# Optimization experiments

Hardware: AMD Instinct MI355X
Metric: run time of the kernel (lower is better)

Reference implementation:

```python
import jax, jax.numpy as jnp
import numpy as np

DIM = 1024
NUM_HEADS = 16
HEAD_DIM = DIM // NUM_HEADS
B, L = 4, 2048


def setup_inputs() -> dict:
    key = jax.random.key(0)
    ks = jax.random.split(key, 7)
    x = jax.random.normal(ks[0], (B, L, DIM), dtype=jnp.float32)
    cos_emb = jax.random.uniform(ks[1], (L, HEAD_DIM), dtype=jnp.float32)
    sin_emb = jax.random.uniform(ks[2], (L, HEAD_DIM), dtype=jnp.float32)
    # nn.Linear params: weight [out, in], bias [out]
    qkv_w = jax.random.normal(ks[3], (3 * DIM, DIM), dtype=jnp.float32) * (DIM ** -0.5)
    qkv_b = jnp.zeros((3 * DIM,), dtype=jnp.float32)
    proj_w = jax.random.normal(ks[4], (DIM, DIM), dtype=jnp.float32) * (DIM ** -0.5)
    proj_b = jnp.zeros((DIM,), dtype=jnp.float32)
    return {"x": x, "cos_emb": cos_emb, "sin_emb": sin_emb,
            "qkv_w": qkv_w, "qkv_b": qkv_b, "proj_w": proj_w, "proj_b": proj_b}


def _rotate_half_interleaved(t):
    # torch.stack([-t[..., 1::2], t[..., ::2]], dim=-1).reshape(t.shape)
    even = t[..., ::2]
    odd = t[..., 1::2]
    return jnp.stack([-odd, even], axis=-1).reshape(t.shape)


def reference(x, cos_emb, sin_emb, qkv_w, qkv_b, proj_w, proj_b):
    b, l, c = x.shape
    h, d = NUM_HEADS, HEAD_DIM
    scale = d ** -0.5
    qkv = x @ qkv_w.T + qkv_b                      # [B, L, 3C]
    qkv = qkv.reshape(b, l, 3, h, d).transpose(2, 0, 3, 1, 4)  # [3, B, H, L, D]
    q, k, v = qkv[0], qkv[1], qkv[2]
    cos = cos_emb[None, None, :l]                  # [1, 1, L, D]
    sin = sin_emb[None, None, :l]
    q = q * cos + _rotate_half_interleaved(q) * sin
    k = k * cos + _rotate_half_interleaved(k) * sin
    attn = scale * jnp.einsum('bhqd,bhkd->bhqk', q, k)  # [B, H, L, L]
    attn = jax.nn.softmax(attn, axis=-1)
    out = jnp.einsum('bhqk,bhkd->bhqd', attn, v)   # [B, H, L, D]
    out = out.transpose(0, 2, 1, 3).reshape(b, l, c)
    return out @ proj_w.T + proj_b
```

## Files before the change

kernel.cpp:

```cpp
#include <hip/hip_runtime.h>
#include <hip/hip_bf16.h>
#include <hip/hip_fp16.h>

#define NHEADS 16
#define HDIM   64
#define BATCH  4
#define SEQ    2048
#define EMB    1024

typedef __attribute__((ext_vector_type(8))) _Float16 f16x8;
typedef __attribute__((ext_vector_type(4))) _Float16 f16x4;
typedef __attribute__((ext_vector_type(2))) __fp16   fp16v2;
typedef __attribute__((ext_vector_type(4))) float  f32x4;
typedef __attribute__((ext_vector_type(4))) unsigned int u32x4;
typedef __attribute__((ext_vector_type(2))) unsigned int u32x2;

#define QSCALE 0.180336884f
#define SSHIFT -8.0f

__device__ __forceinline__ void gload16(const void* g, void* l) {
    __builtin_amdgcn_global_load_lds(
        reinterpret_cast<const __attribute__((address_space(1))) unsigned int*>(
            reinterpret_cast<uintptr_t>(g)),
        reinterpret_cast<__attribute__((address_space(3))) unsigned int*>(
            reinterpret_cast<uintptr_t>(l)),
        16, 0, 0);
}

__global__ __launch_bounds__(256)
void split_pair(const float* __restrict__ in, _Float16* __restrict__ hi,
                _Float16* __restrict__ lo, int n4)
{
    int i = blockIdx.x * 256 + threadIdx.x;
    const int stride = gridDim.x * 256;
    for (; i < n4; i += stride) {
        float4 v = ((const float4*)in)[i];
        f16x4 h, l;
        h[0] = (_Float16)v.x; l[0] = (_Float16)(v.x - (float)h[0]);
        h[1] = (_Float16)v.y; l[1] = (_Float16)(v.y - (float)h[1]);
        h[2] = (_Float16)v.z; l[2] = (_Float16)(v.z - (float)h[2]);
        h[3] = (_Float16)v.w; l[3] = (_Float16)(v.w - (float)h[3]);
        ((f16x4*)hi)[i] = h;
        ((f16x4*)lo)[i] = l;
    }
}

__global__ __launch_bounds__(256)
void split_one(const float* __restrict__ in, _Float16* __restrict__ hi, int n4)
{
    int i = blockIdx.x * 256 + threadIdx.x;
    const int stride = gridDim.x * 256;
    for (; i < n4; i += stride) {
        float4 v = ((const float4*)in)[i];
        f16x4 h;
        h[0] = (_Float16)v.x; h[1] = (_Float16)v.y;
        h[2] = (_Float16)v.z; h[3] = (_Float16)v.w;
        ((f16x4*)hi)[i] = h;
    }
}

template<int EPI, int NX>
__global__ __launch_bounds__(256, 3)
void gemm_f16s(const _Float16* __restrict__ Ah, const _Float16* __restrict__ Al,
               const _Float16* __restrict__ Bh,
               const float* __restrict__ bias, float* __restrict__ C,
               int M, int N, int K,
               const float* __restrict__ cosE, const float* __restrict__ sinE,
               _Float16* __restrict__ qhb, _Float16* __restrict__ qlb,
               _Float16* __restrict__ khb, _Float16* __restrict__ vth)
{
    __shared__ u32x4 AhT[1024], AlT[1024], BhT[1024];

    const int tid  = threadIdx.x;
    const int lane = tid & 63;
    const int w    = tid >> 6;
    const int m16  = lane & 15;
    const int hi4  = lane >> 4;
    const int wr   = w >> 1, wc = w & 1;

    const int lin = blockIdx.x;
    const int cpx = gridDim.x >> 3;
    const int swz = (lin & 7) * cpx + (lin >> 3);
    const int m0  = (swz / NX) * 128;
    const int n0  = (swz % NX) * 128;

    const int lr8 = lane >> 3;
    const int lch = (lane & 7) ^ lr8;

    f32x4 acc[4][4];
#pragma unroll
    for (int i = 0; i < 4; i++)
#pragma unroll
        for (int j = 0; j < 4; j++) acc[i][j] = (f32x4){0.f, 0.f, 0.f, 0.f};

    for (int kt = 0; kt < K; kt += 64) {
        __syncthreads();
#pragma unroll
        for (int c = 0; c < 4; c++) {
            const int rbase = w * 32 + c * 8;
            const size_t ga = (size_t)(m0 + rbase + lr8) * K + kt + lch * 8;
            const size_t gb = (size_t)(n0 + rbase + lr8) * K + kt + lch * 8;
            gload16(Ah + ga, &AhT[rbase * 8]);
            gload16(Al + ga, &AlT[rbase * 8]);
            gload16(Bh + gb, &BhT[rbase * 8]);
        }
        __syncthreads();

#pragma unroll
        for (int kc = 0; kc < 2; kc++) {
            f16x8 fah[4], fal[4], fbh[4];
#pragma unroll
            for (int t = 0; t < 4; t++) {
                const int ra = wr * 64 + t * 16 + m16;
                const int ca = (4 * kc + hi4) ^ (ra & 7);
                fah[t] = *(const f16x8*)&AhT[ra * 8 + ca];
                fal[t] = *(const f16x8*)&AlT[ra * 8 + ca];
                const int rb = wc * 64 + t * 16 + m16;
                const int cb = (4 * kc + hi4) ^ (rb & 7);
                fbh[t] = *(const f16x8*)&BhT[rb * 8 + cb];
            }
#pragma unroll
            for (int i = 0; i < 4; i++)
#pragma unroll
                for (int j = 0; j < 4; j++) {
                    acc[i][j] = __builtin_amdgcn_mfma_f32_16x16x32_f16(fah[i], fbh[j], acc[i][j], 0, 0, 0);
                    acc[i][j] = __builtin_amdgcn_mfma_f32_16x16x32_f16(fal[i], fbh[j], acc[i][j], 0, 0, 0);
                }
        }
    }

    const int nb = n0 + wc * 64;
    if (EPI == 0) {
#pragma unroll
        for (int nt = 0; nt < 4; nt++) {
            const int n = nb + nt * 16 + m16;
            const float bn = bias[n];
#pragma unroll
            for (int mt = 0; mt < 4; mt++) {
                const int m = m0 + wr * 64 + mt * 16 + hi4 * 4;
#pragma unroll
                for (int r = 0; r < 4; r++)
                    C[(size_t)(m + r) * N + n] = acc[mt][nt][r] + bn;
            }
        }
    } else {
        const int which = nb >> 10;
        const int h     = (nb >> 6) & 15;
#pragma unroll
        for (int nt = 0; nt < 4; nt++) {
            const int n  = nb + nt * 16 + m16;
            const int dd = n & 63;
            const float bn = bias[n];
#pragma unroll
            for (int mt = 0; mt < 4; mt++) {
                const int m  = m0 + wr * 64 + mt * 16 + hi4 * 4;
                const int bb = m >> 11;
                const int l  = m & (SEQ - 1);
                const int hb = bb * NHEADS + h;
                if (which == 2) {
                    f16x4 vv;
#pragma unroll
                    for (int r = 0; r < 4; r++)
                        vv[r] = (_Float16)(acc[mt][nt][r] + bn);
                    const size_t vi = ((size_t)(hb * HDIM + dd)) * SEQ + l;
                    *(f16x4*)(vth + vi) = vv;
                } else {
#pragma unroll
                    for (int r = 0; r < 4; r++) {
                        const float v = acc[mt][nt][r] + bn;
                        const float p = __shfl_xor(v, 1);
                        const float cs = cosE[(size_t)(l + r) * HDIM + dd];
                        const float sn = sinE[(size_t)(l + r) * HDIM + dd];
                        float rv = (dd & 1) ? (v * cs + p * sn) : (v * cs - p * sn);
                        const size_t qi = ((size_t)hb * SEQ + l + r) * HDIM + dd;
                        if (which == 0) {
                            rv *= QSCALE;
                            const _Float16 hs = (_Float16)rv;
                            qhb[qi] = hs;
                            qlb[qi] = (_Float16)(rv - (float)hs);
                        } else {
                            khb[qi] = (_Float16)rv;
                        }
                    }
                }
            }
        }
    }
}

__global__ __launch_bounds__(256, 3)
void attn_f16(const _Float16* __restrict__ qh, const _Float16* __restrict__ ql,
              const _Float16* __restrict__ kh, const _Float16* __restrict__ vth,
              _Float16* __restrict__ aoh, _Float16* __restrict__ aol)
{
    __shared__ u32x4 KH[512], VH[512];

    const int tid  = threadIdx.x;
    const int lane = tid & 63;
    const int w    = tid >> 6;
    const int m16  = lane & 15;
    const int hi4  = lane >> 4;

    const int lin = blockIdx.x;
    const int swz = (lin & 7) * 128 + (lin >> 3);
    const int bh  = swz >> 4;
    const int bb  = bh >> 4, h = bh & 15;
    const int q0  = (swz & 15) * 128 + w * 32;

    f16x8 qfh[2][2], qfl[2][2];
#pragma unroll
    for (int s = 0; s < 2; s++) {
        const size_t base = ((size_t)(bh * SEQ + q0 + 16 * s + m16)) * HDIM + hi4 * 8;
#pragma unroll
        for (int c = 0; c < 2; c++) {
            qfh[s][c] = *(const f16x8*)(qh + base + 32 * c);
            qfl[s][c] = *(const f16x8*)(ql + base + 32 * c);
        }
    }

    f32x4 o[2][4];
    float li[2] = {0.f, 0.f};
#pragma unroll
    for (int s = 0; s < 2; s++)
#pragma unroll
        for (int dt = 0; dt < 4; dt++) o[s][dt] = (f32x4){0.f, 0.f, 0.f, 0.f};

    const int srow = tid >> 3;
    const int scc  = tid & 7;

    u32x4 tkh[2], tvh[2];
    auto load_kv = [&](int kt) {
#pragma unroll
        for (int p = 0; p < 2; p++) {
            const int row = srow + p * 32;
            const size_t kg = ((size_t)(bh * SEQ + kt + row)) * HDIM + scc * 8;
            const size_t vg = ((size_t)(bh * HDIM + row)) * SEQ + kt + scc * 8;
            tkh[p] = *(const u32x4*)(kh  + kg);
            tvh[p] = *(const u32x4*)(vth + vg);
        }
    };

    load_kv(0);
    for (int kt = 0; kt < SEQ; kt += 64) {
        __syncthreads();
#pragma unroll
        for (int p = 0; p < 2; p++) {
            const int row = srow + p * 32;
            const int li2 = row * 8 + (scc ^ (row & 7));
            KH[li2] = tkh[p]; VH[li2] = tvh[p];
        }
        __syncthreads();
        if (kt + 64 < SEQ) load_kv(kt + 64);

        f32x4 st[2][4];
#pragma unroll
        for (int s = 0; s < 2; s++)
#pragma unroll
            for (int t = 0; t < 4; t++)
                st[s][t] = (f32x4){SSHIFT, SSHIFT, SSHIFT, SSHIFT};

        __builtin_amdgcn_s_setprio(1);
#pragma unroll
        for (int t = 0; t < 4; t++) {
            const int row = 16 * t + m16;
#pragma unroll
            for (int c = 0; c < 2; c++) {
                const int ch = (4 * c + hi4) ^ (m16 & 7);
                f16x8 ah = *(const f16x8*)&KH[row * 8 + ch];
#pragma unroll
                for (int s = 0; s < 2; s++) {
                    st[s][t] = __builtin_amdgcn_mfma_f32_16x16x32_f16(ah, qfh[s][c], st[s][t], 0, 0, 0);
                    st[s][t] = __builtin_amdgcn_mfma_f32_16x16x32_f16(ah, qfl[s][c], st[s][t], 0, 0, 0);
                }
            }
        }
        __builtin_amdgcn_s_setprio(0);

        f16x8 pb[2][2];
#pragma unroll
        for (int s = 0; s < 2; s++) {
            float rs = 0.f;
#pragma unroll
            for (int t = 0; t < 4; t++)
#pragma unroll
                for (int r = 0; r < 4; r++) {
                    const float pp = __builtin_amdgcn_exp2f(st[s][t][r]);
                    st[s][t][r] = pp;
                    rs += pp;
                }
            rs += __shfl_xor(rs, 16);
            rs += __shfl_xor(rs, 32);
            li[s] += rs;
#pragma unroll
            for (int kc = 0; kc < 2; kc++) {
                union { fp16v2 h2[4]; f16x8 v; } u;
                u.h2[0] = __builtin_amdgcn_cvt_pkrtz(st[s][2*kc][0],   st[s][2*kc][1]);
                u.h2[1] = __builtin_amdgcn_cvt_pkrtz(st[s][2*kc][2],   st[s][2*kc][3]);
                u.h2[2] = __builtin_amdgcn_cvt_pkrtz(st[s][2*kc+1][0], st[s][2*kc+1][1]);
                u.h2[3] = __builtin_amdgcn_cvt_pkrtz(st[s][2*kc+1][2], st[s][2*kc+1][3]);
                pb[s][kc] = u.v;
            }
        }

        const u32x2* VH2 = (const u32x2*)VH;
        __builtin_amdgcn_s_setprio(1);
#pragma unroll
        for (int dt = 0; dt < 4; dt++) {
            const int d   = 16 * dt + m16;
            const int dsw = m16 & 7;
#pragma unroll
            for (int kc = 0; kc < 2; kc++) {
                const int k0a = 32 * kc + 4 * hi4;
                const int k0b = k0a + 16;
                const int ia = (d * 8 + ((k0a >> 3) ^ dsw)) * 2 + ((k0a & 7) >> 2);
                const int ib = (d * 8 + ((k0b >> 3) ^ dsw)) * 2 + ((k0b & 7) >> 2);
                u32x4 th;
                u32x2 a = VH2[ia], b = VH2[ib];
                th.x = a.x; th.y = a.y; th.z = b.x; th.w = b.y;
                f16x8 vhf = *(f16x8*)&th;
#pragma unroll
                for (int s = 0; s < 2; s++)
                    o[s][dt] = __builtin_amdgcn_mfma_f32_16x16x32_f16(vhf, pb[s][kc], o[s][dt], 0, 0, 0);
            }
        }
        __builtin_amdgcn_s_setprio(0);
    }

#pragma unroll
    for (int s = 0; s < 2; s++) {
        const float inv = 1.f / li[s];
        const int q = q0 + 16 * s + m16;
#pragma unroll
        for (int dt = 0; dt < 4; dt++) {
            const f32x4 r = o[s][dt] * inv;
            f16x4 rh, rl;
#pragma unroll
            for (int e = 0; e < 4; e++) {
                rh[e] = (_Float16)r[e];
                rl[e] = (_Float16)(r[e] - (float)rh[e]);
            }
            const size_t idx = ((size_t)(bb * SEQ + q)) * EMB + h * HDIM + 16 * dt + 4 * hi4;
            *(f16x4*)(aoh + idx) = rh;
            *(f16x4*)(aol + idx) = rl;
        }
    }
}

extern "C" void kernel_launch(void* const* d_in, const int* in_sizes, int n_in,
                              void* d_out, int out_size, void* d_ws, size_t ws_size,
                              hipStream_t stream) {
    const float* x      = (const float*)d_in[0];
    const float* cosE   = (const float*)d_in[1];
    const float* sinE   = (const float*)d_in[2];
    const float* qkv_w  = (const float*)d_in[3];
    const float* qkv_b  = (const float*)d_in[4];
    const float* proj_w = (const float*)d_in[5];
    const float* proj_b = (const float*)d_in[6];
    float* out = (float*)d_out;

    char* ws = (char*)d_ws;
    const size_t MB = 1ull << 20;
    _Float16* xh  = (_Float16*)(ws + 0 * MB);
    _Float16* xl  = (_Float16*)(ws + 16 * MB);
    _Float16* qhb = (_Float16*)(ws + 32 * MB);
    _Float16* qlb = (_Float16*)(ws + 48 * MB);
    _Float16* khb = (_Float16*)(ws + 64 * MB);
    _Float16* vth = (_Float16*)(ws + 80 * MB);
    _Float16* qwh = (_Float16*)(ws + 96 * MB);
    _Float16* pwh = (_Float16*)(ws + 102 * MB);

    const int M = BATCH * SEQ;

    split_pair<<<2048, 256, 0, stream>>>(x,      xh,  xl, M * EMB / 4);
    split_one <<<1024, 256, 0, stream>>>(qkv_w,  qwh,     3 * EMB * EMB / 4);
    split_one <<<512,  256, 0, stream>>>(proj_w, pwh,     EMB * EMB / 4);

    gemm_f16s<1, 24><<<1536, 256, 0, stream>>>(xh, xl, qwh, qkv_b, nullptr,
                                               M, 3 * EMB, EMB,
                                               cosE, sinE, qhb, qlb, khb, vth);

    attn_f16<<<1024, 256, 0, stream>>>(qhb, qlb, khb, vth, xh, xl);

    gemm_f16s<0, 8><<<512, 256, 0, stream>>>(xh, xl, pwh, proj_b, out,
                                             M, EMB, EMB,
                                             nullptr, nullptr, nullptr, nullptr,
                                             nullptr, nullptr);
}
```

Baseline: 383.9 us.

## Cut LDS for GEMM low-part, use MFMA row sums, raise occupancy

In the GEMM, the low-half A operand is no longer staged through shared memory. Each wave reads it directly from global memory into registers, which cuts the LDS footprint by a third, and launch bounds rise to 4 waves per SIMD. In attention, the softmax row sum now comes from an MFMA against a vector of ones applied to the fp16 probabilities, replacing the exp-sum plus cross-lane shuffles. The risks are uncoalesced, uncached global loads in the GEMM inner loop, register pressure under the tighter launch bound, and a row sum built from rounded fp16 probabilities.

```diff
diff --git a/kernel.cpp b/kernel.cpp
--- a/kernel.cpp
+++ b/kernel.cpp
@@ -60,7 +60,7 @@
 }
 
 template<int EPI, int NX>
-__global__ __launch_bounds__(256, 3)
+__global__ __launch_bounds__(256, 4)
 void gemm_f16s(const _Float16* __restrict__ Ah, const _Float16* __restrict__ Al,
                const _Float16* __restrict__ Bh,
                const float* __restrict__ bias, float* __restrict__ C,
@@ -69,7 +69,7 @@
                _Float16* __restrict__ qhb, _Float16* __restrict__ qlb,
                _Float16* __restrict__ khb, _Float16* __restrict__ vth)
 {
-    __shared__ u32x4 AhT[1024], AlT[1024], BhT[1024];
+    __shared__ u32x4 AhT[1024], BhT[1024];
 
     const int tid  = threadIdx.x;
     const int lane = tid & 63;
@@ -101,20 +101,27 @@
             const size_t ga = (size_t)(m0 + rbase + lr8) * K + kt + lch * 8;
             const size_t gb = (size_t)(n0 + rbase + lr8) * K + kt + lch * 8;
             gload16(Ah + ga, &AhT[rbase * 8]);
-            gload16(Al + ga, &AlT[rbase * 8]);
             gload16(Bh + gb, &BhT[rbase * 8]);
         }
         __syncthreads();
 
+        f16x8 fal[2][4];
+#pragma unroll
+        for (int kc = 0; kc < 2; kc++)
+#pragma unroll
+            for (int t = 0; t < 4; t++) {
+                const int ra = m0 + wr * 64 + t * 16 + m16;
+                fal[kc][t] = *(const f16x8*)(Al + (size_t)ra * K + kt + kc * 32 + hi4 * 8);
+            }
+
 #pragma unroll
         for (int kc = 0; kc < 2; kc++) {
-            f16x8 fah[4], fal[4], fbh[4];
+            f16x8 fah[4], fbh[4];
 #pragma unroll
             for (int t = 0; t < 4; t++) {
                 const int ra = wr * 64 + t * 16 + m16;
                 const int ca = (4 * kc + hi4) ^ (ra & 7);
                 fah[t] = *(const f16x8*)&AhT[ra * 8 + ca];
-                fal[t] = *(const f16x8*)&AlT[ra * 8 + ca];
                 const int rb = wc * 64 + t * 16 + m16;
                 const int cb = (4 * kc + hi4) ^ (rb & 7);
                 fbh[t] = *(const f16x8*)&BhT[rb * 8 + cb];
@@ -122,10 +129,13 @@
 #pragma unroll
             for (int i = 0; i < 4; i++)
 #pragma unroll
-                for (int j = 0; j < 4; j++) {
+                for (int j = 0; j < 4; j++)
                     acc[i][j] = __builtin_amdgcn_mfma_f32_16x16x32_f16(fah[i], fbh[j], acc[i][j], 0, 0, 0);
-                    acc[i][j] = __builtin_amdgcn_mfma_f32_16x16x32_f16(fal[i], fbh[j], acc[i][j], 0, 0, 0);
-                }
+#pragma unroll
+            for (int i = 0; i < 4; i++)
+#pragma unroll
+                for (int j = 0; j < 4; j++)
+                    acc[i][j] = __builtin_amdgcn_mfma_f32_16x16x32_f16(fal[kc][i], fbh[j], acc[i][j], 0, 0, 0);
         }
     }
 
@@ -188,7 +198,7 @@
     }
 }
 
-__global__ __launch_bounds__(256, 3)
+__global__ __launch_bounds__(256, 4)
 void attn_f16(const _Float16* __restrict__ qh, const _Float16* __restrict__ ql,
               const _Float16* __restrict__ kh, const _Float16* __restrict__ vth,
               _Float16* __restrict__ aoh, _Float16* __restrict__ aol)
@@ -218,12 +228,17 @@
         }
     }
 
-    f32x4 o[2][4];
-    float li[2] = {0.f, 0.f};
-#pragma unroll
-    for (int s = 0; s < 2; s++)
+    f16x8 vones;
+#pragma unroll
+    for (int e = 0; e < 8; e++) vones[e] = (_Float16)1.0f;
+
+    f32x4 o[2][4], acc_li[2];
+#pragma unroll
+    for (int s = 0; s < 2; s++) {
+        acc_li[s] = (f32x4){0.f, 0.f, 0.f, 0.f};
 #pragma unroll
         for (int dt = 0; dt < 4; dt++) o[s][dt] = (f32x4){0.f, 0.f, 0.f, 0.f};
+    }
 
     const int srow = tid >> 3;
     const int scc  = tid & 7;
@@ -279,18 +294,11 @@
         f16x8 pb[2][2];
 #pragma unroll
         for (int s = 0; s < 2; s++) {
-            float rs = 0.f;
 #pragma unroll
             for (int t = 0; t < 4; t++)
 #pragma unroll
-                for (int r = 0; r < 4; r++) {
-                    const float pp = __builtin_amdgcn_exp2f(st[s][t][r]);
-                    st[s][t][r] = pp;
-                    rs += pp;
-                }
-            rs += __shfl_xor(rs, 16);
-            rs += __shfl_xor(rs, 32);
-            li[s] += rs;
+                for (int r = 0; r < 4; r++)
+                    st[s][t][r] = __builtin_amdgcn_exp2f(st[s][t][r]);
 #pragma unroll
             for (int kc = 0; kc < 2; kc++) {
                 union { fp16v2 h2[4]; f16x8 v; } u;
@@ -304,6 +312,11 @@
 
         const u32x2* VH2 = (const u32x2*)VH;
         __builtin_amdgcn_s_setprio(1);
+#pragma unroll
+        for (int s = 0; s < 2; s++)
+#pragma unroll
+            for (int kc = 0; kc < 2; kc++)
+                acc_li[s] = __builtin_amdgcn_mfma_f32_16x16x32_f16(vones, pb[s][kc], acc_li[s], 0, 0, 0);
 #pragma unroll
         for (int dt = 0; dt < 4; dt++) {
             const int d   = 16 * dt + m16;
@@ -328,7 +341,7 @@
 
 #pragma unroll
     for (int s = 0; s < 2; s++) {
-        const float inv = 1.f / li[s];
+        const float inv = 1.f / acc_li[s][0];
         const int q = q0 + 16 * s + m16;
 #pragma unroll
         for (int dt = 0; dt < 4; dt++) {
```

Result: slower. 644.9 us (+68.0%).
